# Optimization experiments

Hardware: AMD Instinct MI355X
Metric: run time of the kernel (lower is better)

The kernel has to match this reference:

```python
import jax, jax.numpy as jnp
import numpy as np

NUM_HEADS = 16


def setup_inputs() -> dict:
    key = jax.random.key(0)
    k1, k2, k3, k4 = jax.random.split(key, 4)
    B, N, C = 8, 1024, 1024
    x = jax.random.normal(k1, (B, N, C), dtype=jnp.float32)
    # torch Linear weights are [out_features, in_features]
    w_qkv = jax.random.normal(k2, (3 * C, C), dtype=jnp.float32) * (C ** -0.5)
    w_proj = jax.random.normal(k3, (C, C), dtype=jnp.float32) * (C ** -0.5)
    b_proj = jax.random.normal(k4, (C,), dtype=jnp.float32) * 0.01
    return {"x": x, "w_qkv": w_qkv, "w_proj": w_proj, "b_proj": b_proj}


def reference(x, w_qkv, w_proj, b_proj):
    B, N, C = x.shape
    H = NUM_HEADS
    D = C // H
    scale = D ** -0.5  # attn_scale MulShift (bias=0)
    # xq / qqkv / qproj quantizers and qkv_deq MulShift are identity in train mode
    qkv = jnp.einsum('bnc,fc->bnf', x, w_qkv)           # [B, N, 3C] (no bias)
    qkv = qkv.reshape(B, N, 3, H, D).transpose(2, 0, 3, 1, 4)  # [3, B, H, N, D]
    q, k, v = qkv[0], qkv[1], qkv[2]
    attn = jnp.einsum('bhqd,bhkd->bhqk', q, k) * scale  # [B, H, N, N]
    attn = jax.nn.softmax(attn, axis=-1)
    out = jnp.einsum('bhqk,bhkd->bhqd', attn, v)        # [B, H, N, D]
    out = out.transpose(0, 2, 1, 3).reshape(B, N, C)
    out = jnp.einsum('bnc,fc->bnf', out, w_proj) + b_proj
    return out
```

## Files before the change

kernel.cpp:

```cpp
#include <hip/hip_runtime.h>

typedef unsigned short u16;
typedef unsigned int u32;
typedef unsigned long long u64;

typedef __attribute__((ext_vector_type(8))) short short8;
typedef __attribute__((ext_vector_type(2))) float f32x2;
typedef __attribute__((ext_vector_type(4))) float f32x4;
typedef __attribute__((ext_vector_type(16))) float f32x16;
typedef __attribute__((ext_vector_type(4))) u32 u32x4;

#define DEVI static __device__ __forceinline__

DEVI u16 f2bf(float f) {
  u32 u = __float_as_uint(f);
  return (u16)((u + 0x7fffu + ((u >> 16) & 1u)) >> 16);
}

DEVI u64 pack4f(float a, float b, float c, float d) {
  return (u64)f2bf(a) | ((u64)f2bf(b) << 16) | ((u64)f2bf(c) << 32) |
         ((u64)f2bf(d) << 48);
}

DEVI u32 cvtpk_bf16(float lo, float hi) {
  u32 r;
  asm("v_cvt_pk_bf16_f32 %0, %1, %2" : "=v"(r) : "v"(lo), "v"(hi));
  return r;
}

DEVI void gld_lds16(const void* g, void* l) {
  __builtin_amdgcn_global_load_lds(
      (const __attribute__((address_space(1))) void*)g,
      (__attribute__((address_space(3))) void*)l, 16, 0, 0);
}

DEVI f32x4 mfma16(short8 a, short8 b, f32x4 c) {
  return __builtin_amdgcn_mfma_f32_16x16x32_bf16(a, b, c, 0, 0, 0);
}

DEVI f32x16 mfma32(short8 a, short8 b, f32x16 c) {
  return __builtin_amdgcn_mfma_f32_32x32x16_bf16(a, b, c, 0, 0, 0);
}

DEVI f32x4 zero4() {
  f32x4 z = {0.f, 0.f, 0.f, 0.f};
  return z;
}

__global__ __launch_bounds__(256) void cvt_all(const float* __restrict__ x,
                                               const float* __restrict__ wq,
                                               const float* __restrict__ wp,
                                               u16* __restrict__ xb,
                                               u16* __restrict__ wqb,
                                               u16* __restrict__ wpb) {
  const int NX = 2097152, NQ = 786432, NP = 262144;
  int i = blockIdx.x * 256 + threadIdx.x;
  const int stride = gridDim.x * 256;
  for (; i < NX + NQ + NP; i += stride) {
    const float* s;
    u16* d;
    int j;
    if (i < NX) {
      s = x; d = xb; j = i;
    } else if (i < NX + NQ) {
      s = wq; d = wqb; j = i - NX;
    } else {
      s = wp; d = wpb; j = i - NX - NQ;
    }
    f32x4 v = ((const f32x4*)s)[j];
    ((u64*)d)[j] = pack4f(v.x, v.y, v.z, v.w);
  }
}

__global__ __launch_bounds__(256, 2) void gemm_qkv_impl(
    const u16* __restrict__ W, const u16* __restrict__ X, u16* __restrict__ Q,
    u16* __restrict__ K, u16* __restrict__ V) {
  __shared__ alignas(16) char smem[36864];
  u16* As = (u16*)smem;
  u16* Bs = (u16*)(smem + 16384);

  const int tid = threadIdx.x;
  const int wid = tid >> 6, lane = tid & 63;
  const int lr = lane & 15, lg = lane >> 4;
  const int wr = wid >> 1, wc = wid & 1;

  const int f_base = blockIdx.y * 128;
  const int m_base = blockIdx.x * 128;

  f32x4 acc[4][4];
#pragma unroll
  for (int i = 0; i < 4; ++i)
#pragma unroll
    for (int j = 0; j < 4; ++j) acc[i][j] = zero4();

  const int grow = tid >> 3;
  const int gch = tid & 7;
  const int gsw = gch ^ (grow & 7);
  const u64 soff = (u64)grow * 2048 + gsw * 16;
  const char* Ag = (const char*)(W + (u64)f_base * 1024) + soff;
  const char* Bg = (const char*)(X + (u64)m_base * 1024) + soff;
  char* Asd = (char*)As + tid * 16;
  char* Bsd = (char*)Bs + tid * 16;

  int aoff[2][4], boff[2][4];
#pragma unroll
  for (int kk = 0; kk < 2; ++kk)
#pragma unroll
    for (int i = 0; i < 4; ++i) {
      int ra = wr * 64 + i * 16 + lr;
      int rb = wc * 64 + i * 16 + lr;
      aoff[kk][i] = ra * 128 + (((kk * 4 + lg) ^ (ra & 7)) << 4);
      boff[kk][i] = rb * 128 + (((kk * 4 + lg) ^ (rb & 7)) << 4);
    }

  for (int kt = 0; kt < 16; ++kt) {
    const u64 kb = (u64)kt * 128;
#pragma unroll
    for (int i = 0; i < 4; ++i) {
      gld_lds16(Ag + kb + (u64)i * 65536, Asd + i * 4096);
      gld_lds16(Bg + kb + (u64)i * 65536, Bsd + i * 4096);
    }
    __syncthreads();
    short8 af[2][4], bf[2][4];
#pragma unroll
    for (int kk = 0; kk < 2; ++kk) {
#pragma unroll
      for (int i = 0; i < 4; ++i) {
        af[kk][i] = *(const short8*)((const char*)As + aoff[kk][i]);
        bf[kk][i] = *(const short8*)((const char*)Bs + boff[kk][i]);
      }
    }
    __builtin_amdgcn_s_setprio(1);
#pragma unroll
    for (int kk = 0; kk < 2; ++kk)
#pragma unroll
      for (int mi = 0; mi < 4; ++mi)
#pragma unroll
        for (int ni = 0; ni < 4; ++ni)
          acc[mi][ni] = mfma16(af[kk][mi], bf[kk][ni], acc[mi][ni]);
    __builtin_amdgcn_s_setprio(0);
    __syncthreads();
  }

  const int f0 = f_base + wr * 64;
  const int m0 = m_base + wc * 64;
  const int b = m0 >> 10, n0 = m0 & 1023;
  const int which = f0 >> 10;
  const int h = (f0 & 1023) >> 6;
  const int bh = b * 16 + h;

  if (which < 2) {
    const float qs = (which == 0) ? (0.125f * 1.44269504088896f) : 1.f;
    u16* Ob = (u16*)smem + wid * (64 * 72);
#pragma unroll
    for (int mi = 0; mi < 4; ++mi)
#pragma unroll
      for (int ni = 0; ni < 4; ++ni) {
        int ml = ni * 16 + lr;
        int fl = mi * 16 + lg * 4;
        f32x4 a = acc[mi][ni] * qs;
        *(u64*)(Ob + ml * 72 + fl) = pack4f(a.x, a.y, a.z, a.w);
      }
    __syncthreads();
    u16* dst = (which ? K : Q) + ((u64)bh * 1024 + n0) * 64;
#pragma unroll
    for (int it = 0; it < 8; ++it) {
      int ml = it * 8 + (lane >> 3);
      int c = lane & 7;
      *(short8*)(dst + ml * 64 + c * 8) = *(const short8*)(Ob + ml * 72 + c * 8);
    }
  } else {
    u16* dst = V + (u64)bh * 64 * 1024;
    const int lrp = (lr & 3) | ((lr & 4) << 1) | ((lr & 8) >> 1);
#pragma unroll
    for (int mi = 0; mi < 4; ++mi) {
      int d0 = mi * 16 + lg * 4;
#pragma unroll
      for (int ni = 0; ni < 4; ++ni) {
        int n = n0 + ni * 16 + lrp;
#pragma unroll
        for (int r = 0; r < 4; ++r)
          dst[(u64)(d0 + r) * 1024 + n] = f2bf(acc[mi][ni][r]);
      }
    }
  }
}

__global__ __launch_bounds__(512, 4) void attn_fwd(const u16* __restrict__ Q,
                                                   const u16* __restrict__ K,
                                                   const u16* __restrict__ V,
                                                   u16* __restrict__ AO) {
  __shared__ alignas(16) char smem[65536];
  char* Ks0 = smem;
  char* Vs0 = smem + 32768;

  const int tid = threadIdx.x;
  const int wid = tid >> 6, lane = tid & 63;
  const int l31 = lane & 31, hi = lane >> 5;

  const int i = blockIdx.x;
  const int qblk = (i >> 3) & 3;
  const int bh = (i & 7) * 16 + (i >> 5);

  const u64 kvbase = (u64)bh * (1024 * 64);
  const int q0w = qblk * 256 + wid * 32;

  short8 qf[4];
  {
    const char* qrow = (const char*)(Q + kvbase + (u64)(q0w + l31) * 64);
#pragma unroll
    for (int ss = 0; ss < 4; ++ss)
      qf[ss] = *(const short8*)(qrow + 32 * ss + 16 * hi);
  }

  float l_run = 0.f;
  f32x16 o0 = {0}, o1 = {0};

  const int sr = tid & 63;
  const int sc0 = (tid >> 6) & 3;
  const int sh = tid >> 8;
  const char* kgb = (const char*)(K + kvbase);
  const char* vgb = (const char*)(V + kvbase);

#define STAGE(buf, kt)                                                       \
  do {                                                                       \
    const char* kg = kgb + (u64)(kt) * 16384 + (sh * 64 + sr) * 128;         \
    const char* vg = vgb + (kt) * 256 + sh * 128 + sr * 2048;                \
    char* kd = Ks0 + (buf) * 16384 + sh * 8192 + sr * 16;                    \
    char* vd = Vs0 + (buf) * 16384 + sh * 8192 + sr * 16;                    \
    gld_lds16(kg + sc0 * 16, kd + sc0 * 1024);                               \
    gld_lds16(kg + (sc0 + 4) * 16, kd + (sc0 + 4) * 1024);                   \
    gld_lds16(vg + sc0 * 16, vd + sc0 * 1024);                               \
    gld_lds16(vg + (sc0 + 4) * 16, vd + (sc0 + 4) * 1024);                   \
  } while (0)

  STAGE(0, 0);

  struct F2x8 { f32x2 h[8]; };

  for (int kt = 0; kt < 8; ++kt) {
    const int cur = kt & 1;
    if (kt + 1 < 8) {
      STAGE(cur ^ 1, kt + 1);
      asm volatile("s_waitcnt vmcnt(4)" ::: "memory");
    } else {
      asm volatile("s_waitcnt vmcnt(0)" ::: "memory");
    }
    __builtin_amdgcn_s_barrier();
    asm volatile("" ::: "memory");

#pragma unroll
    for (int hh = 0; hh < 2; ++hh) {
      const char* Kc = Ks0 + cur * 16384 + hh * 8192;
      const char* Vc = Vs0 + cur * 16384 + hh * 8192;

      f32x16 s0 = {0}, s1 = {0};
      __builtin_amdgcn_s_setprio(1);
#pragma unroll
      for (int ss = 0; ss < 4; ++ss) {
        const int ch = (2 * ss + hi) << 10;
        short8 kf0 = *(const short8*)(Kc + ch + (l31 << 4));
        short8 kf1 = *(const short8*)(Kc + ch + ((32 + l31) << 4));
        s0 = mfma32(kf0, qf[ss], s0);
        s1 = mfma32(kf1, qf[ss], s1);
      }
      __builtin_amdgcn_s_setprio(0);

#pragma unroll
      for (int j = 0; j < 16; ++j) {
        s0[j] = exp2f(s0[j]);
        s1[j] = exp2f(s1[j]);
      }
      F2x8 a0 = __builtin_bit_cast(F2x8, s0);
      F2x8 a1 = __builtin_bit_cast(F2x8, s1);
      f32x2 t0 = (a0.h[0] + a0.h[1]) + (a0.h[2] + a0.h[3]);
      f32x2 t1 = (a0.h[4] + a0.h[5]) + (a0.h[6] + a0.h[7]);
      f32x2 t2 = (a1.h[0] + a1.h[1]) + (a1.h[2] + a1.h[3]);
      f32x2 t3 = (a1.h[4] + a1.h[5]) + (a1.h[6] + a1.h[7]);
      f32x2 tt = (t0 + t1) + (t2 + t3);
      float psum = tt.x + tt.y;
      psum += __shfl_xor(psum, 32);
      l_run += psum;

      __builtin_amdgcn_s_setprio(1);
#pragma unroll
      for (int s = 0; s < 4; ++s) {
        const int off = (s & 1) * 8;
        u32x4 pw;
        if (s < 2) {
          pw.x = cvtpk_bf16(s0[off + 0], s0[off + 1]);
          pw.y = cvtpk_bf16(s0[off + 2], s0[off + 3]);
          pw.z = cvtpk_bf16(s0[off + 4], s0[off + 5]);
          pw.w = cvtpk_bf16(s0[off + 6], s0[off + 7]);
        } else {
          pw.x = cvtpk_bf16(s1[off + 0], s1[off + 1]);
          pw.y = cvtpk_bf16(s1[off + 2], s1[off + 3]);
          pw.z = cvtpk_bf16(s1[off + 4], s1[off + 5]);
          pw.w = cvtpk_bf16(s1[off + 6], s1[off + 7]);
        }
        short8 pf = __builtin_bit_cast(short8, pw);

        const int ch = (2 * s + hi) << 10;
        short8 vf0 = *(const short8*)(Vc + ch + (l31 << 4));
        short8 vf1 = *(const short8*)(Vc + ch + ((32 + l31) << 4));
        o0 = mfma32(vf0, pf, o0);
        o1 = mfma32(vf1, pf, o1);
      }
      __builtin_amdgcn_s_setprio(0);
    }

    asm volatile("" ::: "memory");
    __builtin_amdgcn_s_barrier();
    asm volatile("" ::: "memory");
  }
#undef STAGE

  __syncthreads();
  float inv_l = 1.f / l_run;
  u16* Ob = (u16*)(smem + wid * 4096);
#pragma unroll
  for (int j4 = 0; j4 < 4; ++j4) {
    u64 wa = (u64)cvtpk_bf16(o0[4 * j4] * inv_l, o0[4 * j4 + 1] * inv_l) |
             ((u64)cvtpk_bf16(o0[4 * j4 + 2] * inv_l, o0[4 * j4 + 3] * inv_l)
              << 32);
    u64 wb = (u64)cvtpk_bf16(o1[4 * j4] * inv_l, o1[4 * j4 + 1] * inv_l) |
             ((u64)cvtpk_bf16(o1[4 * j4 + 2] * inv_l, o1[4 * j4 + 3] * inv_l)
              << 32);
    *(u64*)(Ob + l31 * 64 + (((j4 ^ (l31 & 7)) << 4) + 8 * hi) / 2) = wa;
    *(u64*)(Ob + l31 * 64 + ((((4 + j4) ^ (l31 & 7)) << 4) + 8 * hi) / 2) = wb;
  }
  const int b = bh >> 4, h = bh & 15;
#pragma unroll
  for (int it = 0; it < 4; ++it) {
    int qr = it * 8 + (lane >> 3);
    int cd = lane & 7;
    short8 vvv = *(const short8*)(Ob + qr * 64 + (((cd ^ (qr & 7)) << 4) / 2));
    u16* dst = AO + ((u64)(b * 1024 + q0w + qr) * 1024 + h * 64 + cd * 8);
    *(short8*)dst = vvv;
  }
}

__global__ __launch_bounds__(256, 2) void gemm_proj(const u16* __restrict__ W,
                                                    const u16* __restrict__ X,
                                                    const float* __restrict__ bias,
                                                    float* __restrict__ Out) {
  __shared__ alignas(16) char smem[32768];
  u16* As = (u16*)smem;
  u16* Bs = (u16*)(smem + 16384);

  const int tid = threadIdx.x;
  const int wid = tid >> 6, lane = tid & 63;
  const int lr = lane & 15, lg = lane >> 4;
  const int wr = wid >> 1, wc = wid & 1;

  const int f_base = blockIdx.y * 128;
  const int m_base = blockIdx.x * 128;

  f32x4 acc[4][4];
#pragma unroll
  for (int i = 0; i < 4; ++i)
#pragma unroll
    for (int j = 0; j < 4; ++j) acc[i][j] = zero4();

  const int grow = tid >> 3;
  const int gch = tid & 7;
  const int gsw = gch ^ (grow & 7);
  const u64 soff = (u64)grow * 2048 + gsw * 16;
  const char* Ag = (const char*)(W + (u64)f_base * 1024) + soff;
  const char* Bg = (const char*)(X + (u64)m_base * 1024) + soff;
  char* Asd = (char*)As + tid * 16;
  char* Bsd = (char*)Bs + tid * 16;

  int aoff[2][4], boff[2][4];
#pragma unroll
  for (int kk = 0; kk < 2; ++kk)
#pragma unroll
    for (int i = 0; i < 4; ++i) {
      int ra = wr * 64 + i * 16 + lr;
      int rb = wc * 64 + i * 16 + lr;
      aoff[kk][i] = ra * 128 + (((kk * 4 + lg) ^ (ra & 7)) << 4);
      boff[kk][i] = rb * 128 + (((kk * 4 + lg) ^ (rb & 7)) << 4);
    }

  for (int kt = 0; kt < 16; ++kt) {
    const u64 kb = (u64)kt * 128;
#pragma unroll
    for (int i = 0; i < 4; ++i) {
      gld_lds16(Ag + kb + (u64)i * 65536, Asd + i * 4096);
      gld_lds16(Bg + kb + (u64)i * 65536, Bsd + i * 4096);
    }
    __syncthreads();
    short8 af[2][4], bf[2][4];
#pragma unroll
    for (int kk = 0; kk < 2; ++kk) {
#pragma unroll
      for (int i = 0; i < 4; ++i) {
        af[kk][i] = *(const short8*)((const char*)As + aoff[kk][i]);
        bf[kk][i] = *(const short8*)((const char*)Bs + boff[kk][i]);
      }
    }
    __builtin_amdgcn_s_setprio(1);
#pragma unroll
    for (int kk = 0; kk < 2; ++kk)
#pragma unroll
      for (int mi = 0; mi < 4; ++mi)
#pragma unroll
        for (int ni = 0; ni < 4; ++ni)
          acc[mi][ni] = mfma16(af[kk][mi], bf[kk][ni], acc[mi][ni]);
    __builtin_amdgcn_s_setprio(0);
    __syncthreads();
  }

  const int f0 = f_base + wr * 64;
  const int m0 = m_base + wc * 64;
#pragma unroll
  for (int mi = 0; mi < 4; ++mi) {
    int f = f0 + mi * 16 + lg * 4;
    f32x4 bv = *(const f32x4*)(bias + f);
#pragma unroll
    for (int ni = 0; ni < 4; ++ni) {
      int m = m0 + ni * 16 + lr;
      f32x4 o = acc[mi][ni] + bv;
      *(f32x4*)(Out + (u64)m * 1024 + f) = o;
    }
  }
}

extern "C" void kernel_launch(void* const* d_in, const int* in_sizes, int n_in,
                              void* d_out, int out_size, void* d_ws,
                              size_t ws_size, hipStream_t stream) {
  const float* x = (const float*)d_in[0];
  const float* w_qkv = (const float*)d_in[1];
  const float* w_proj = (const float*)d_in[2];
  const float* b_proj = (const float*)d_in[3];
  float* out = (float*)d_out;
  char* ws = (char*)d_ws;

  u16* xb = (u16*)(ws);
  u16* wqb = (u16*)(ws + 16777216);
  u16* wpb = (u16*)(ws + 23068672);
  u16* qb = (u16*)(ws + 25165824);
  u16* kb = (u16*)(ws + 41943040);
  u16* vt = (u16*)(ws + 58720256);
  u16* ao = (u16*)(ws + 75497472);

  hipLaunchKernelGGL(cvt_all, dim3(2048), dim3(256), 0, stream, x, w_qkv,
                     w_proj, xb, wqb, wpb);
  hipLaunchKernelGGL(gemm_qkv_impl, dim3(64, 24), dim3(256), 0, stream, wqb,
                     xb, qb, kb, vt);
  hipLaunchKernelGGL(attn_fwd, dim3(512), dim3(512), 0, stream, qb, kb, vt,
                     ao);
  hipLaunchKernelGGL(gemm_proj, dim3(64, 8), dim3(256), 0, stream, wpb, ao,
                     b_proj, out);
}
```

Before: 138.8 us.

## Double-buffer LDS tiles in QKV and projection GEMMs to overlap loads with MFMA

Both GEMM kernels now use two LDS buffers per operand and issue the global-to-LDS loads for the next K tile before computing on the current one. Explicit vmcnt waits plus raw barriers replace the full __syncthreads pairs. The aim is to hide global memory latency behind MFMA work. LDS per block rises to 64KB, which with launch_bounds of 2 blocks uses the whole 128KB and may limit occupancy.

```diff
diff --git a/kernel.cpp b/kernel.cpp
--- a/kernel.cpp
+++ b/kernel.cpp
@@ -75,9 +75,7 @@
 __global__ __launch_bounds__(256, 2) void gemm_qkv_impl(
     const u16* __restrict__ W, const u16* __restrict__ X, u16* __restrict__ Q,
     u16* __restrict__ K, u16* __restrict__ V) {
-  __shared__ alignas(16) char smem[36864];
-  u16* As = (u16*)smem;
-  u16* Bs = (u16*)(smem + 16384);
+  __shared__ alignas(16) char smem[65536];
 
   const int tid = threadIdx.x;
   const int wid = tid >> 6, lane = tid & 63;
@@ -99,8 +97,6 @@
   const u64 soff = (u64)grow * 2048 + gsw * 16;
   const char* Ag = (const char*)(W + (u64)f_base * 1024) + soff;
   const char* Bg = (const char*)(X + (u64)m_base * 1024) + soff;
-  char* Asd = (char*)As + tid * 16;
-  char* Bsd = (char*)Bs + tid * 16;
 
   int aoff[2][4], boff[2][4];
 #pragma unroll
@@ -113,21 +109,39 @@
       boff[kk][i] = rb * 128 + (((kk * 4 + lg) ^ (rb & 7)) << 4);
     }
 
+#define GSTAGE(buf, kt)                                                      \
+  do {                                                                       \
+    const u64 kb = (u64)(kt) * 128;                                          \
+    char* Ad = smem + (buf) * 16384 + tid * 16;                              \
+    char* Bd = smem + 32768 + (buf) * 16384 + tid * 16;                      \
+    _Pragma("unroll") for (int i = 0; i < 4; ++i) {                          \
+      gld_lds16(Ag + kb + (u64)i * 65536, Ad + i * 4096);                    \
+      gld_lds16(Bg + kb + (u64)i * 65536, Bd + i * 4096);                    \
+    }                                                                        \
+  } while (0)
+
+  GSTAGE(0, 0);
+
   for (int kt = 0; kt < 16; ++kt) {
-    const u64 kb = (u64)kt * 128;
-#pragma unroll
-    for (int i = 0; i < 4; ++i) {
-      gld_lds16(Ag + kb + (u64)i * 65536, Asd + i * 4096);
-      gld_lds16(Bg + kb + (u64)i * 65536, Bsd + i * 4096);
-    }
-    __syncthreads();
+    const int cur = kt & 1;
+    if (kt + 1 < 16) {
+      GSTAGE(cur ^ 1, kt + 1);
+      asm volatile("s_waitcnt vmcnt(8)" ::: "memory");
+    } else {
+      asm volatile("s_waitcnt vmcnt(0)" ::: "memory");
+    }
+    __builtin_amdgcn_s_barrier();
+    asm volatile("" ::: "memory");
+
+    const char* Ab = smem + cur * 16384;
+    const char* Bb = smem + 32768 + cur * 16384;
     short8 af[2][4], bf[2][4];
 #pragma unroll
     for (int kk = 0; kk < 2; ++kk) {
 #pragma unroll
       for (int i = 0; i < 4; ++i) {
-        af[kk][i] = *(const short8*)((const char*)As + aoff[kk][i]);
-        bf[kk][i] = *(const short8*)((const char*)Bs + boff[kk][i]);
+        af[kk][i] = *(const short8*)(Ab + aoff[kk][i]);
+        bf[kk][i] = *(const short8*)(Bb + boff[kk][i]);
       }
     }
     __builtin_amdgcn_s_setprio(1);
@@ -139,8 +153,12 @@
         for (int ni = 0; ni < 4; ++ni)
           acc[mi][ni] = mfma16(af[kk][mi], bf[kk][ni], acc[mi][ni]);
     __builtin_amdgcn_s_setprio(0);
-    __syncthreads();
-  }
+
+    asm volatile("" ::: "memory");
+    __builtin_amdgcn_s_barrier();
+    asm volatile("" ::: "memory");
+  }
+#undef GSTAGE
 
   const int f0 = f_base + wr * 64;
   const int m0 = m_base + wc * 64;
@@ -152,6 +170,7 @@
   if (which < 2) {
     const float qs = (which == 0) ? (0.125f * 1.44269504088896f) : 1.f;
     u16* Ob = (u16*)smem + wid * (64 * 72);
+    __syncthreads();
 #pragma unroll
     for (int mi = 0; mi < 4; ++mi)
 #pragma unroll
@@ -344,9 +363,7 @@
                                                     const u16* __restrict__ X,
                                                     const float* __restrict__ bias,
                                                     float* __restrict__ Out) {
-  __shared__ alignas(16) char smem[32768];
-  u16* As = (u16*)smem;
-  u16* Bs = (u16*)(smem + 16384);
+  __shared__ alignas(16) char smem[65536];
 
   const int tid = threadIdx.x;
   const int wid = tid >> 6, lane = tid & 63;
@@ -368,8 +385,6 @@
   const u64 soff = (u64)grow * 2048 + gsw * 16;
   const char* Ag = (const char*)(W + (u64)f_base * 1024) + soff;
   const char* Bg = (const char*)(X + (u64)m_base * 1024) + soff;
-  char* Asd = (char*)As + tid * 16;
-  char* Bsd = (char*)Bs + tid * 16;
 
   int aoff[2][4], boff[2][4];
 #pragma unroll
@@ -382,21 +397,39 @@
       boff[kk][i] = rb * 128 + (((kk * 4 + lg) ^ (rb & 7)) << 4);
     }
 
+#define GSTAGE(buf, kt)                                                      \
+  do {                                                                       \
+    const u64 kb = (u64)(kt) * 128;                                          \
+    char* Ad = smem + (buf) * 16384 + tid * 16;                              \
+    char* Bd = smem + 32768 + (buf) * 16384 + tid * 16;                      \
+    _Pragma("unroll") for (int i = 0; i < 4; ++i) {                          \
+      gld_lds16(Ag + kb + (u64)i * 65536, Ad + i * 4096);                    \
+      gld_lds16(Bg + kb + (u64)i * 65536, Bd + i * 4096);                    \
+    }                                                                        \
+  } while (0)
+
+  GSTAGE(0, 0);
+
   for (int kt = 0; kt < 16; ++kt) {
-    const u64 kb = (u64)kt * 128;
-#pragma unroll
-    for (int i = 0; i < 4; ++i) {
-      gld_lds16(Ag + kb + (u64)i * 65536, Asd + i * 4096);
-      gld_lds16(Bg + kb + (u64)i * 65536, Bsd + i * 4096);
-    }
-    __syncthreads();
+    const int cur = kt & 1;
+    if (kt + 1 < 16) {
+      GSTAGE(cur ^ 1, kt + 1);
+      asm volatile("s_waitcnt vmcnt(8)" ::: "memory");
+    } else {
+      asm volatile("s_waitcnt vmcnt(0)" ::: "memory");
+    }
+    __builtin_amdgcn_s_barrier();
+    asm volatile("" ::: "memory");
+
+    const char* Ab = smem + cur * 16384;
+    const char* Bb = smem + 32768 + cur * 16384;
     short8 af[2][4], bf[2][4];
 #pragma unroll
     for (int kk = 0; kk < 2; ++kk) {
 #pragma unroll
       for (int i = 0; i < 4; ++i) {
-        af[kk][i] = *(const short8*)((const char*)As + aoff[kk][i]);
-        bf[kk][i] = *(const short8*)((const char*)Bs + boff[kk][i]);
+        af[kk][i] = *(const short8*)(Ab + aoff[kk][i]);
+        bf[kk][i] = *(const short8*)(Bb + boff[kk][i]);
       }
     }
     __builtin_amdgcn_s_setprio(1);
@@ -408,8 +441,12 @@
         for (int ni = 0; ni < 4; ++ni)
           acc[mi][ni] = mfma16(af[kk][mi], bf[kk][ni], acc[mi][ni]);
     __builtin_amdgcn_s_setprio(0);
-    __syncthreads();
-  }
+
+    asm volatile("" ::: "memory");
+    __builtin_amdgcn_s_barrier();
+    asm volatile("" ::: "memory");
+  }
+#undef GSTAGE
 
   const int f0 = f_base + wr * 64;
   const int m0 = m_base + wc * 64;
```

New measurement: 138.4 us. No clear change (-0.3%).
